# Kernel tuning notes

Measured on AMD Instinct MI355X. Metric: run time of the kernel, lower is better.

## Reference

```python
import jax, jax.numpy as jnp
import numpy as np

EMBED_DIM = 1024
NUM_HEADS = 16
HEAD_DIM = EMBED_DIM // NUM_HEADS
B, N = 2, 2048
BIAS_S = 32


def _interp_matrix(n, s):
    # Bilinear interpolation (align_corners=True) along one axis as an (n, s) matrix.
    pos = jnp.arange(n, dtype=jnp.float32) * ((s - 1) / (n - 1))
    i0 = jnp.floor(pos).astype(jnp.int32)
    i1 = jnp.minimum(i0 + 1, s - 1)
    frac = pos - i0.astype(jnp.float32)
    rows = jnp.arange(n)
    M = jnp.zeros((n, s), dtype=jnp.float32)
    M = M.at[rows, i0].add(1.0 - frac).at[rows, i1].add(frac)
    return M


def setup_inputs() -> dict:
    key = jax.random.key(0)
    ks = jax.random.split(key, 12)
    std = 0.02
    d = {
        'x': jax.random.normal(ks[0], (B, N, EMBED_DIM), dtype=jnp.float32),
        'Wq': jax.random.normal(ks[1], (EMBED_DIM, EMBED_DIM), dtype=jnp.float32) * std,
        'bq': jnp.zeros((EMBED_DIM,), dtype=jnp.float32),
        'Wk': jax.random.normal(ks[2], (EMBED_DIM, EMBED_DIM), dtype=jnp.float32) * std,
        'bk': jnp.zeros((EMBED_DIM,), dtype=jnp.float32),
        'Wv': jax.random.normal(ks[3], (EMBED_DIM, EMBED_DIM), dtype=jnp.float32) * std,
        'bv': jnp.zeros((EMBED_DIM,), dtype=jnp.float32),
        'Wo': jax.random.normal(ks[4], (EMBED_DIM, EMBED_DIM), dtype=jnp.float32) * std,
        'bo': jnp.zeros((EMBED_DIM,), dtype=jnp.float32),
        'gamma': jnp.ones((EMBED_DIM,), dtype=jnp.float32),
        'beta': jnp.zeros((EMBED_DIM,), dtype=jnp.float32),
        'rel_bias': jax.random.normal(ks[5], (NUM_HEADS, BIAS_S, BIAS_S), dtype=jnp.float32) * std,
    }
    return d


def reference(x, Wq, bq, Wk, bk, Wv, bv, Wo, bo, gamma, beta, rel_bias):
    Bx, Nx, C = x.shape
    H, D = NUM_HEADS, HEAD_DIM
    scale = 1.0 / jnp.sqrt(jnp.float32(D))

    # LayerNorm
    mu = jnp.mean(x, axis=-1, keepdims=True)
    var = jnp.mean(jnp.square(x - mu), axis=-1, keepdims=True)
    xn = (x - mu) * jax.lax.rsqrt(var + 1e-5) * gamma + beta

    q = (xn @ Wq.T + bq).reshape(Bx, Nx, H, D).transpose(0, 2, 1, 3)
    k = (xn @ Wk.T + bk).reshape(Bx, Nx, H, D).transpose(0, 2, 1, 3)
    v = (xn @ Wv.T + bv).reshape(Bx, Nx, H, D).transpose(0, 2, 1, 3)

    attn = jnp.einsum('bhnd,bhmd->bhnm', q, k) * scale  # [B,H,N,N]

    # Bilinear interp of rel_pos_bias (H,32,32) -> (H,N,N), align_corners=True
    M = _interp_matrix(Nx, BIAS_S)  # (N, 32)
    rel = jnp.einsum('ni,hij,mj->hnm', M, rel_bias, M)
    rel = rel.at[:, -1, :].set(0.0).at[:, :, -1].set(0.0)
    attn = attn + rel[None]

    mask = jnp.triu(jnp.ones((Nx, Nx), dtype=bool), k=1)
    attn = jnp.where(mask, -jnp.inf, attn)
    attn = jax.nn.softmax(attn, axis=-1)

    out = jnp.einsum('bhnm,bhmd->bhnd', attn, v)
    out = out.transpose(0, 2, 1, 3).reshape(Bx, Nx, C)
    out = out @ Wo.T + bo  # dropout is identity in eval mode
    return out
```

## Files before the change

### kernel.cpp

```cpp
#include <hip/hip_runtime.h>
#include <hip/hip_bf16.h>

#define EMBED 1024
#define NHEADS 16
#define HDIM 64
#define NB 2
#define NSEQ 2048
#define NTOK (NB*NSEQ)

using short8  = __attribute__((ext_vector_type(8))) short;
using short4v = __attribute__((ext_vector_type(4))) short;
using f32x4   = __attribute__((ext_vector_type(4))) float;

#define INV_LN2 1.4426950408889634f

__device__ __forceinline__ short f2bf(float x) {
  __hip_bfloat16 h = __float2bfloat16(x);
  short s;
  __builtin_memcpy(&s, &h, 2);
  return s;
}

#define GLDS16(gp, lp) __builtin_amdgcn_global_load_lds( \
    (const __attribute__((address_space(1))) unsigned int*)(const void*)(gp), \
    (__attribute__((address_space(3))) unsigned int*)(void*)(lp), 16, 0, 0)

__global__ __launch_bounds__(256) void ln_kernel(const float* __restrict__ x,
    const float* __restrict__ gamma, const float* __restrict__ beta,
    short* __restrict__ xn) {
  const int row = blockIdx.x;
  const int tid = threadIdx.x;
  const float* xr = x + (size_t)row * EMBED;
  float4 v = *(const float4*)(xr + tid * 4);
  float s  = v.x + v.y + v.z + v.w;
  float s2 = v.x*v.x + v.y*v.y + v.z*v.z + v.w*v.w;
#pragma unroll
  for (int off = 32; off; off >>= 1) {
    s  += __shfl_down(s, off);
    s2 += __shfl_down(s2, off);
  }
  __shared__ float red[8];
  const int wv = tid >> 6, ln = tid & 63;
  if (ln == 0) { red[wv] = s; red[4 + wv] = s2; }
  __syncthreads();
  s  = red[0] + red[1] + red[2] + red[3];
  s2 = red[4] + red[5] + red[6] + red[7];
  const float mu  = s * (1.0f / EMBED);
  const float var = s2 * (1.0f / EMBED) - mu * mu;
  const float inv = rsqrtf(var + 1e-5f);
  float4 g  = *(const float4*)(gamma + tid * 4);
  float4 bt = *(const float4*)(beta + tid * 4);
  short4v o;
  o[0] = f2bf((v.x - mu) * inv * g.x + bt.x);
  o[1] = f2bf((v.y - mu) * inv * g.y + bt.y);
  o[2] = f2bf((v.z - mu) * inv * g.z + bt.z);
  o[3] = f2bf((v.w - mu) * inv * g.w + bt.w);
  *(short4v*)(xn + (size_t)row * EMBED + tid * 4) = o;
}

__global__ __launch_bounds__(256) void cast4_kernel(
    const float* __restrict__ a, const float* __restrict__ b,
    const float* __restrict__ c, const float* __restrict__ d,
    short* __restrict__ oa, short* __restrict__ ob,
    short* __restrict__ oc, short* __restrict__ od) {
  const int wsel = blockIdx.y;
  const float* s = (wsel == 0) ? a : (wsel == 1) ? b : (wsel == 2) ? c : d;
  short* o       = (wsel == 0) ? oa : (wsel == 1) ? ob : (wsel == 2) ? oc : od;
  const int i = (blockIdx.x * 256 + threadIdx.x) * 4;
  float4 v = *(const float4*)(s + i);
  short4v r;
  r[0] = f2bf(v.x); r[1] = f2bf(v.y); r[2] = f2bf(v.z); r[3] = f2bf(v.w);
  *(short4v*)(o + i) = r;
}

template<bool F32OUT>
__global__ __launch_bounds__(256) void gemm_kernel(
    const short* __restrict__ A,
    const short* __restrict__ W0, const short* __restrict__ W1, const short* __restrict__ W2,
    const float* __restrict__ b0, const float* __restrict__ b1, const float* __restrict__ b2,
    void* __restrict__ O0, void* __restrict__ O1, void* __restrict__ O2) {
  constexpr int K = 1024, NOUT = 1024;
  const int z = blockIdx.z;
  const short* Bw   = (z == 0) ? W0 : (z == 1) ? W1 : W2;
  const float* bias = (z == 0) ? b0 : (z == 1) ? b1 : b2;
  void* Cout        = (z == 0) ? O0 : (z == 1) ? O1 : O2;

  const int tn = blockIdx.x, tm = blockIdx.y;
  const int tid = threadIdx.x, w = tid >> 6, lane = tid & 63;
  const int wm = w >> 1, wn = w & 1;
  const int g = lane >> 4, c = lane & 15;

  __shared__ short As[128 * 32];
  __shared__ short Bs[128 * 32];

  f32x4 acc[4][4];
#pragma unroll
  for (int i = 0; i < 4; i++)
#pragma unroll
    for (int j = 0; j < 4; j++) acc[i][j] = (f32x4){0.f, 0.f, 0.f, 0.f};

  const int crow = tid >> 2;
  const int ckc  = tid & 3;
  const short* ga = A  + (size_t)(tm * 128 + crow) * K + ckc * 8;
  const short* gb = Bw + (size_t)(tn * 128 + crow) * K + ckc * 8;
  short* la = &As[tid * 8];
  short* lb = &Bs[tid * 8];

  for (int k0 = 0; k0 < K; k0 += 32) {
    __syncthreads();
    GLDS16(ga + k0, la);
    GLDS16(ga + k0 + (size_t)64 * K, la + 64 * 32);
    GLDS16(gb + k0, lb);
    GLDS16(gb + k0 + (size_t)64 * K, lb + 64 * 32);
    __syncthreads();
    short8 af[4], bfr[4];
#pragma unroll
    for (int mi = 0; mi < 4; mi++)
      af[mi] = *(const short8*)&As[(wm * 64 + mi * 16 + c) * 32 + g * 8];
#pragma unroll
    for (int ni = 0; ni < 4; ni++)
      bfr[ni] = *(const short8*)&Bs[(wn * 64 + ni * 16 + c) * 32 + g * 8];
#pragma unroll
    for (int mi = 0; mi < 4; mi++)
#pragma unroll
      for (int ni = 0; ni < 4; ni++)
        acc[mi][ni] = __builtin_amdgcn_mfma_f32_16x16x32_bf16(af[mi], bfr[ni], acc[mi][ni], 0, 0, 0);
  }

#pragma unroll
  for (int ni = 0; ni < 4; ni++) {
    const int col = tn * 128 + wn * 64 + ni * 16 + c;
    const float bs = bias[col];
#pragma unroll
    for (int mi = 0; mi < 4; mi++) {
#pragma unroll
      for (int j = 0; j < 4; j++) {
        const int row = tm * 128 + wm * 64 + mi * 16 + g * 4 + j;
        const float v = acc[mi][ni][j] + bs;
        if constexpr (F32OUT)
          ((float*)Cout)[(size_t)row * NOUT + col] = v;
        else
          ((short*)Cout)[(size_t)row * NOUT + col] = f2bf(v);
      }
    }
  }
}

__global__ __launch_bounds__(256) void vtrans_kernel(const short* __restrict__ vb,
                                                     short* __restrict__ vt) {
  const int n0 = blockIdx.x * 64;
  const int bh = blockIdx.y;
  const int b = bh >> 4, h = bh & 15;
  const int tid = threadIdx.x;
  __shared__ short tl[64 * 68];

  const int r  = tid >> 3;
  const int c8 = (tid & 7) * 8;
#pragma unroll
  for (int i = 0; i < 2; i++) {
    const int row = r + i * 32;
    short8 v = *(const short8*)(vb + (size_t)(b * NSEQ + n0 + row) * EMBED + h * 64 + c8);
    *(short8*)&tl[row * 68 + c8] = v;
  }
  __syncthreads();
  const int d  = tid >> 2;
  const int ns = (tid & 3) * 16;
  short8 o0, o1;
#pragma unroll
  for (int e = 0; e < 8; e++) {
    o0[e] = tl[(ns + e) * 68 + d];
    o1[e] = tl[(ns + 8 + e) * 68 + d];
  }
  short* dst = vt + ((size_t)((b * 16 + h) * 64 + d)) * 2048 + n0 + ns;
  *(short8*)dst = o0;
  *(short8*)(dst + 8) = o1;
}

__global__ __launch_bounds__(512, 4) void attn_kernel(
    const short* __restrict__ Qm, const short* __restrict__ Km, const short* __restrict__ Vt,
    const float* __restrict__ relb, short* __restrict__ ctx) {
  const int bid = blockIdx.x;
  const int bh  = bid & 31;
  const int idx = bid >> 5;
  const int qpair = (idx < 8) ? (15 - idx) : (idx - 8);
  const int b = bh >> 4, h = bh & 15;
  const int tid = threadIdx.x, w = tid >> 6, lane = tid & 63;
  const int g = lane >> 4, c = lane & 15;
  constexpr float S31 = 31.0f / 2047.0f;
  constexpr float CSC = 0.125f * INV_LN2;

  __shared__ short k_lds[2][64 * 64];
  __shared__ short vt_lds[2][64 * 64];
  __shared__ short p_lds[8][16 * 64];
  __shared__ short rbf[128 * 32];
  __shared__ short u_lds[2][64 * 40];

  const int qbase = qpair * 128;
  const size_t bhq = (size_t)b * NSEQ * EMBED + h * HDIM;
  const short* vtb = Vt + (size_t)((b << 4) + h) * 64 * 2048;

  short8 qf[2];
  {
    const short* qp = Qm + bhq + (size_t)(qbase + w * 16 + c) * EMBED;
    qf[0] = *(const short8*)(qp + g * 8);
    qf[1] = *(const short8*)(qp + 32 + g * 8);
  }

  const int srow = tid >> 3;
  const int sd0  = (tid & 7) * 8;
  const int swz  = (srow & 7) << 3;

  auto buildU = [&](int buf, int kv) {
    if (tid < 64) {
      short* ur = &u_lds[buf][tid * 40];
      *(int4*)&ur[0]  = (int4){0, 0, 0, 0};
      *(int4*)&ur[8]  = (int4){0, 0, 0, 0};
      *(int4*)&ur[16] = (int4){0, 0, 0, 0};
      *(int4*)&ur[24] = (int4){0, 0, 0, 0};
      const int m = kv + tid;
      if (m != NSEQ - 1) {
        const float pos = m * S31;
        const int i0 = (int)pos;
        const float fr = pos - (float)i0;
        ur[i0]     = f2bf(1.0f - fr);
        ur[i0 + 1] = f2bf(fr);
      }
    }
  };

  GLDS16(Km + bhq + (size_t)srow * EMBED + (sd0 ^ swz), &k_lds[0][srow * 64 + sd0]);
  GLDS16(vtb + (size_t)srow * 2048 + (sd0 ^ swz),       &vt_lds[0][srow * 64 + sd0]);
  for (int i = tid; i < 128 * 32; i += 512) {
    const int qr = i >> 5, jj = i & 31;
    const int qg0 = qbase + qr;
    float rv = 0.f;
    if (qg0 != NSEQ - 1) {
      const float pos = qg0 * S31;
      const int i0 = (int)pos;
      const int i1 = min(i0 + 1, 31);
      const float fr = pos - (float)i0;
      const float* T = relb + h * 1024;
      rv = ((1.f - fr) * T[i0 * 32 + jj] + fr * T[i1 * 32 + jj]) * 8.0f;
    }
    rbf[i] = f2bf(rv);
  }
  buildU(0, 0);
  __syncthreads();

  const short8 rq = *(const short8*)&rbf[(w * 16 + c) * 32 + g * 8];

  float mrow = -3.0e38f, lrow = 0.f;
  f32x4 oacc[4];
#pragma unroll
  for (int db = 0; db < 4; db++) oacc[db] = (f32x4){0.f, 0.f, 0.f, 0.f};

  const int qg  = qbase + w * 16 + c;
  const int qhi = qbase + w * 16 + 15;
  const int csw = (c & 7) << 3;
  const int nkv = 2 * qpair + 2;

  for (int kt = 0; kt < nkv; kt++) {
    const int cur = kt & 1;
    const int kv0 = kt * 64;

    if (kt + 1 < nkv) {
      GLDS16(Km + bhq + (size_t)(kv0 + 64 + srow) * EMBED + (sd0 ^ swz),
             &k_lds[cur ^ 1][srow * 64 + sd0]);
      GLDS16(vtb + (size_t)srow * 2048 + (kv0 + 64) + (sd0 ^ swz),
             &vt_lds[cur ^ 1][srow * 64 + sd0]);
      buildU(cur ^ 1, kv0 + 64);
    }

    if (kv0 <= qhi) {
      const short* kl = &k_lds[cur][0];
      const short* vl = &vt_lds[cur][0];
      const short* ul = &u_lds[cur][0];

      f32x4 st[4];
#pragma unroll
      for (int mb = 0; mb < 4; mb++) st[mb] = (f32x4){0.f, 0.f, 0.f, 0.f};
      __builtin_amdgcn_s_setprio(1);
#pragma unroll
      for (int kh = 0; kh < 2; kh++) {
        const int dk = kh * 32 + g * 8;
#pragma unroll
        for (int mb = 0; mb < 4; mb++) {
          const int row = mb * 16 + c;
          short8 kf = *(const short8*)&kl[row * 64 + (dk ^ ((row & 7) << 3))];
          st[mb] = __builtin_amdgcn_mfma_f32_16x16x32_bf16(kf, qf[kh], st[mb], 0, 0, 0);
        }
      }
#pragma unroll
      for (int mb = 0; mb < 4; mb++) {
        short8 uf = *(const short8*)&ul[(mb * 16 + c) * 40 + g * 8];
        st[mb] = __builtin_amdgcn_mfma_f32_16x16x32_bf16(uf, rq, st[mb], 0, 0, 0);
      }
      __builtin_amdgcn_s_setprio(0);

      const bool diag = (kv0 + 63 > qg);
      if (diag) {
#pragma unroll
        for (int mb = 0; mb < 4; mb++)
#pragma unroll
          for (int j = 0; j < 4; j++) {
            const int mg = kv0 + mb * 16 + g * 4 + j;
            if (mg > qg) st[mb][j] = -1.0e38f;
          }
      }
      float pmr = -3.0e38f;
#pragma unroll
      for (int mb = 0; mb < 4; mb++)
#pragma unroll
        for (int j = 0; j < 4; j++) pmr = fmaxf(pmr, st[mb][j]);
      float pmax = pmr * CSC;
      pmax = fmaxf(pmax, __shfl_xor(pmax, 16));
      pmax = fmaxf(pmax, __shfl_xor(pmax, 32));

      if (!__all(pmax - mrow <= 11.6f)) {
        const float mnew = fmaxf(mrow, pmax);
        const float al = exp2f(mrow - mnew);
        mrow = mnew;
        lrow *= al;
        float alj[4];
#pragma unroll
        for (int j = 0; j < 4; j++) alj[j] = __shfl(al, g * 4 + j);
#pragma unroll
        for (int db = 0; db < 4; db++)
#pragma unroll
          for (int j = 0; j < 4; j++) oacc[db][j] *= alj[j];
      }

      float p[4][4];
      float rs = 0.f;
#pragma unroll
      for (int mb = 0; mb < 4; mb++)
#pragma unroll
        for (int j = 0; j < 4; j++) {
          const float pe = exp2f(fmaf(st[mb][j], CSC, -mrow));
          p[mb][j] = pe;
          rs += pe;
        }
      rs += __shfl_xor(rs, 16);
      rs += __shfl_xor(rs, 32);
      lrow += rs;

      short* pw = &p_lds[w][0];
#pragma unroll
      for (int mb = 0; mb < 4; mb++)
#pragma unroll
        for (int jh = 0; jh < 2; jh++) {
          const int m = mb * 16 + g * 4 + jh * 2;
          unsigned int pk = ((unsigned int)(unsigned short)f2bf(p[mb][jh * 2 + 1]) << 16)
                          |  (unsigned int)(unsigned short)f2bf(p[mb][jh * 2]);
          *(unsigned int*)&pw[c * 64 + (m ^ csw)] = pk;
        }

      __builtin_amdgcn_s_setprio(1);
#pragma unroll
      for (int kb = 0; kb < 2; kb++) {
        const int m0 = kb * 32 + g * 8;
        short8 pa = *(const short8*)&pw[c * 64 + (m0 ^ csw)];
#pragma unroll
        for (int db = 0; db < 4; db++) {
          const int d = db * 16 + c;
          short8 vf = *(const short8*)&vl[d * 64 + (m0 ^ ((d & 7) << 3))];
          oacc[db] = __builtin_amdgcn_mfma_f32_16x16x32_bf16(pa, vf, oacc[db], 0, 0, 0);
        }
      }
      __builtin_amdgcn_s_setprio(0);
    }
    __syncthreads();
  }

  float linv[4];
#pragma unroll
  for (int j = 0; j < 4; j++) linv[j] = 1.f / __shfl(lrow, g * 4 + j);
#pragma unroll
  for (int j = 0; j < 4; j++) {
    short* op = ctx + bhq + (size_t)(qbase + w * 16 + g * 4 + j) * EMBED;
#pragma unroll
    for (int db = 0; db < 4; db++)
      op[db * 16 + c] = f2bf(oacc[db][j] * linv[j]);
  }
}

extern "C" void kernel_launch(void* const* d_in, const int* in_sizes, int n_in,
                              void* d_out, int out_size, void* d_ws, size_t ws_size,
                              hipStream_t stream) {
  const float* x     = (const float*)d_in[0];
  const float* Wq    = (const float*)d_in[1];
  const float* bq    = (const float*)d_in[2];
  const float* Wk    = (const float*)d_in[3];
  const float* bk    = (const float*)d_in[4];
  const float* Wv    = (const float*)d_in[5];
  const float* bv    = (const float*)d_in[6];
  const float* Wo    = (const float*)d_in[7];
  const float* bo    = (const float*)d_in[8];
  const float* gamma = (const float*)d_in[9];
  const float* beta  = (const float*)d_in[10];
  const float* relb  = (const float*)d_in[11];
  float* out = (float*)d_out;

  char* ws = (char*)d_ws;
  short* xn  = (short*)ws; ws += (size_t)NTOK * EMBED * 2;
  short* wqb = (short*)ws; ws += (size_t)EMBED * EMBED * 2;
  short* wkb = (short*)ws; ws += (size_t)EMBED * EMBED * 2;
  short* wvb = (short*)ws; ws += (size_t)EMBED * EMBED * 2;
  short* wob = (short*)ws; ws += (size_t)EMBED * EMBED * 2;
  short* qb  = (short*)ws; ws += (size_t)NTOK * EMBED * 2;
  short* kb_ = (short*)ws; ws += (size_t)NTOK * EMBED * 2;
  short* vb  = (short*)ws; ws += (size_t)NTOK * EMBED * 2;
  short* ctx = (short*)ws; ws += (size_t)NTOK * EMBED * 2;
  short* vtb = xn;

  ln_kernel<<<dim3(NTOK), dim3(256), 0, stream>>>(x, gamma, beta, xn);
  cast4_kernel<<<dim3(1024, 4), dim3(256), 0, stream>>>(Wq, Wk, Wv, Wo, wqb, wkb, wvb, wob);
  gemm_kernel<false><<<dim3(8, 32, 3), dim3(256), 0, stream>>>(
      xn, wqb, wkb, wvb, bq, bk, bv, (void*)qb, (void*)kb_, (void*)vb);
  vtrans_kernel<<<dim3(32, 32), dim3(256), 0, stream>>>(vb, vtb);
  attn_kernel<<<dim3(512), dim3(512), 0, stream>>>(qb, kb_, vtb, relb, ctx);
  gemm_kernel<true><<<dim3(8, 32, 1), dim3(256), 0, stream>>>(
      ctx, wob, wob, wob, bo, bo, bo, (void*)out, (void*)out, (void*)out);
}
```

Measured before the change: 217.7 us.

## Fuse LayerNorm with weight casts and add a pipelined 256x256 QKV GEMM

Merges the LayerNorm and weight bf16-cast kernels into one launch. Replaces the 128x128 QKV GEMM with a 512-thread, 256x256-tile kernel. The new kernel double-buffers LDS using direct global-to-LDS loads with XOR swizzling, interleaves MFMA phases with s_setprio, and applies a block-index swizzle. The larger tile raises arithmetic intensity and hides load latency, but it needs 128KB of LDS and launches only 192 blocks, which may underfill the GPU's CUs.

```diff
diff --git a/kernel.cpp b/kernel.cpp
--- a/kernel.cpp
+++ b/kernel.cpp
@@ -25,66 +25,200 @@
     (const __attribute__((address_space(1))) unsigned int*)(const void*)(gp), \
     (__attribute__((address_space(3))) unsigned int*)(void*)(lp), 16, 0, 0)
 
-__global__ __launch_bounds__(256) void ln_kernel(const float* __restrict__ x,
-    const float* __restrict__ gamma, const float* __restrict__ beta,
-    short* __restrict__ xn) {
-  const int row = blockIdx.x;
+#define BAR() __builtin_amdgcn_s_barrier()
+#define WAITVM(N) asm volatile("s_waitcnt vmcnt(" #N ")" ::: "memory")
+#define PH_SYNC1() do { BAR(); \
+    asm volatile("s_waitcnt lgkmcnt(0)" ::: "memory"); \
+    __builtin_amdgcn_sched_barrier(0); \
+    __builtin_amdgcn_s_setprio(1); } while (0)
+#define PH_SYNC2() do { __builtin_amdgcn_s_setprio(0); BAR(); } while (0)
+
+__global__ __launch_bounds__(256) void lncast_kernel(const float* __restrict__ x,
+    const float* __restrict__ gamma, const float* __restrict__ beta, short* __restrict__ xn,
+    const float* __restrict__ Wq, const float* __restrict__ Wk,
+    const float* __restrict__ Wv, const float* __restrict__ Wo,
+    short* __restrict__ wqb, short* __restrict__ wkb,
+    short* __restrict__ wvb, short* __restrict__ wob) {
+  const int bid = blockIdx.x;
   const int tid = threadIdx.x;
-  const float* xr = x + (size_t)row * EMBED;
-  float4 v = *(const float4*)(xr + tid * 4);
-  float s  = v.x + v.y + v.z + v.w;
-  float s2 = v.x*v.x + v.y*v.y + v.z*v.z + v.w*v.w;
-#pragma unroll
-  for (int off = 32; off; off >>= 1) {
-    s  += __shfl_down(s, off);
-    s2 += __shfl_down(s2, off);
-  }
-  __shared__ float red[8];
-  const int wv = tid >> 6, ln = tid & 63;
-  if (ln == 0) { red[wv] = s; red[4 + wv] = s2; }
-  __syncthreads();
-  s  = red[0] + red[1] + red[2] + red[3];
-  s2 = red[4] + red[5] + red[6] + red[7];
-  const float mu  = s * (1.0f / EMBED);
-  const float var = s2 * (1.0f / EMBED) - mu * mu;
-  const float inv = rsqrtf(var + 1e-5f);
-  float4 g  = *(const float4*)(gamma + tid * 4);
-  float4 bt = *(const float4*)(beta + tid * 4);
-  short4v o;
-  o[0] = f2bf((v.x - mu) * inv * g.x + bt.x);
-  o[1] = f2bf((v.y - mu) * inv * g.y + bt.y);
-  o[2] = f2bf((v.z - mu) * inv * g.z + bt.z);
-  o[3] = f2bf((v.w - mu) * inv * g.w + bt.w);
-  *(short4v*)(xn + (size_t)row * EMBED + tid * 4) = o;
-}
-
-__global__ __launch_bounds__(256) void cast4_kernel(
-    const float* __restrict__ a, const float* __restrict__ b,
-    const float* __restrict__ c, const float* __restrict__ d,
-    short* __restrict__ oa, short* __restrict__ ob,
-    short* __restrict__ oc, short* __restrict__ od) {
-  const int wsel = blockIdx.y;
-  const float* s = (wsel == 0) ? a : (wsel == 1) ? b : (wsel == 2) ? c : d;
-  short* o       = (wsel == 0) ? oa : (wsel == 1) ? ob : (wsel == 2) ? oc : od;
-  const int i = (blockIdx.x * 256 + threadIdx.x) * 4;
-  float4 v = *(const float4*)(s + i);
-  short4v r;
-  r[0] = f2bf(v.x); r[1] = f2bf(v.y); r[2] = f2bf(v.z); r[3] = f2bf(v.w);
-  *(short4v*)(o + i) = r;
-}
-
-template<bool F32OUT>
-__global__ __launch_bounds__(256) void gemm_kernel(
+  if (bid < NTOK) {
+    const float* xr = x + (size_t)bid * EMBED;
+    float4 v = *(const float4*)(xr + tid * 4);
+    float s  = v.x + v.y + v.z + v.w;
+    float s2 = v.x*v.x + v.y*v.y + v.z*v.z + v.w*v.w;
+#pragma unroll
+    for (int off = 32; off; off >>= 1) {
+      s  += __shfl_down(s, off);
+      s2 += __shfl_down(s2, off);
+    }
+    __shared__ float red[8];
+    const int wv = tid >> 6, ln = tid & 63;
+    if (ln == 0) { red[wv] = s; red[4 + wv] = s2; }
+    __syncthreads();
+    s  = red[0] + red[1] + red[2] + red[3];
+    s2 = red[4] + red[5] + red[6] + red[7];
+    const float mu  = s * (1.0f / EMBED);
+    const float var = s2 * (1.0f / EMBED) - mu * mu;
+    const float inv = rsqrtf(var + 1e-5f);
+    float4 g  = *(const float4*)(gamma + tid * 4);
+    float4 bt = *(const float4*)(beta + tid * 4);
+    short4v o;
+    o[0] = f2bf((v.x - mu) * inv * g.x + bt.x);
+    o[1] = f2bf((v.y - mu) * inv * g.y + bt.y);
+    o[2] = f2bf((v.z - mu) * inv * g.z + bt.z);
+    o[3] = f2bf((v.w - mu) * inv * g.w + bt.w);
+    *(short4v*)(xn + (size_t)bid * EMBED + tid * 4) = o;
+  } else {
+    const int i = (bid - NTOK) * 1024 + tid * 4;
+    const int wsel = i >> 20;
+    const int off  = i & 1048575;
+    const float* s = (wsel == 0) ? Wq : (wsel == 1) ? Wk : (wsel == 2) ? Wv : Wo;
+    short* o       = (wsel == 0) ? wqb : (wsel == 1) ? wkb : (wsel == 2) ? wvb : wob;
+    float4 v = *(const float4*)(s + off);
+    short4v r;
+    r[0] = f2bf(v.x); r[1] = f2bf(v.y); r[2] = f2bf(v.z); r[3] = f2bf(v.w);
+    *(short4v*)(o + off) = r;
+  }
+}
+
+__global__ __launch_bounds__(512, 2) void qkv8_kernel(
     const short* __restrict__ A,
     const short* __restrict__ W0, const short* __restrict__ W1, const short* __restrict__ W2,
     const float* __restrict__ b0, const float* __restrict__ b1, const float* __restrict__ b2,
-    void* __restrict__ O0, void* __restrict__ O1, void* __restrict__ O2) {
+    short* __restrict__ O0, short* __restrict__ O1, short* __restrict__ O2) {
+  constexpr int K = 1024;
+  const int orig = blockIdx.x;
+  const int swzb = (orig & 7) * 24 + (orig >> 3);
+  const int tn = swzb % 12, tm = swzb / 12;
+  const int sel = tn >> 2;
+  const short* Bw   = (sel == 0) ? W0 : (sel == 1) ? W1 : W2;
+  const float* bias = (sel == 0) ? b0 : (sel == 1) ? b1 : b2;
+  short* Cout       = (sel == 0) ? O0 : (sel == 1) ? O1 : O2;
+  const int ncol0 = (tn & 3) * 256;
+
+  const int tid = threadIdx.x;
+  const int w = tid >> 6, lane = tid & 63;
+  const int wr = w >> 2, wc = w & 3;
+  const int g = lane >> 4, c = lane & 15;
+
+  __shared__ short As[2][256 * 64];
+  __shared__ short Bs[2][256 * 64];
+
+  f32x4 acc[8][4];
+#pragma unroll
+  for (int i = 0; i < 8; i++)
+#pragma unroll
+    for (int j = 0; j < 4; j++) acc[i][j] = (f32x4){0.f, 0.f, 0.f, 0.f};
+
+  const int sr  = tid >> 3;
+  const int sc8 = (tid & 7) * 8;
+  const int ssw = (sr & 7) << 3;
+  const short* ga = A  + (size_t)(tm * 256) * K;
+  const short* gb = Bw + (size_t)ncol0 * K;
+
+  auto stA = [&](int buf, int h, int kt) {
+#pragma unroll
+    for (int i = 0; i < 2; i++) {
+      const int row = h * 64 + i * 128 + sr;
+      GLDS16(ga + (size_t)row * K + kt * 64 + (sc8 ^ ssw), &As[buf][row * 64 + sc8]);
+    }
+  };
+  auto stB = [&](int buf, int h, int kt) {
+#pragma unroll
+    for (int i = 0; i < 2; i++) {
+      const int row = ((sr >> 5) + 2 * i) * 64 + (sr & 31) + h * 32;
+      GLDS16(gb + (size_t)row * K + kt * 64 + (sc8 ^ ssw), &Bs[buf][row * 64 + sc8]);
+    }
+  };
+
+  short8 af[4][2], bf[4][2];
+  auto ldA = [&](const short* as, int mh) {
+#pragma unroll
+    for (int mi = 0; mi < 4; mi++) {
+      const int row = wr * 128 + mh * 64 + mi * 16 + c;
+      const int sw = (row & 7) << 3;
+#pragma unroll
+      for (int ks = 0; ks < 2; ks++)
+        af[mi][ks] = *(const short8*)&as[row * 64 + ((ks * 32 + g * 8) ^ sw)];
+    }
+  };
+  auto ldB = [&](const short* bs) {
+#pragma unroll
+    for (int ni = 0; ni < 4; ni++) {
+      const int row = wc * 64 + ni * 16 + c;
+      const int sw = (row & 7) << 3;
+#pragma unroll
+      for (int ks = 0; ks < 2; ks++)
+        bf[ni][ks] = *(const short8*)&bs[row * 64 + ((ks * 32 + g * 8) ^ sw)];
+    }
+  };
+  auto MF = [&](int mh, int nh) {
+#pragma unroll
+    for (int ks = 0; ks < 2; ks++)
+#pragma unroll
+      for (int mi = 0; mi < 4; mi++)
+#pragma unroll
+        for (int ni = 0; ni < 2; ni++)
+          acc[mh * 4 + mi][nh * 2 + ni] = __builtin_amdgcn_mfma_f32_16x16x32_bf16(
+              af[mi][ks], bf[nh * 2 + ni][ks], acc[mh * 4 + mi][nh * 2 + ni], 0, 0, 0);
+  };
+
+  stA(0, 0, 0); stB(0, 0, 0); stA(0, 1, 0); stB(0, 1, 0);
+  stA(1, 0, 1); stB(1, 0, 1);
+  WAITVM(4);
+  BAR();
+
+  for (int i = 0; i < 8; ++i) {
+    const bool pre = (i < 7);
+    const int e2 = 2 * i + 2, o1 = 2 * i + 1, o3 = 2 * i + 3;
+    ldA(As[0], 0); ldB(Bs[0]);
+    stA(1, 1, o1);
+    PH_SYNC1(); MF(0, 0); PH_SYNC2();
+    stB(1, 1, o1);
+    PH_SYNC1(); MF(0, 1); PH_SYNC2();
+    ldA(As[0], 1);
+    if (pre) stA(0, 0, e2);
+    PH_SYNC1(); MF(1, 0); PH_SYNC2();
+    if (pre) stB(0, 0, e2);
+    PH_SYNC1(); MF(1, 1);
+    __builtin_amdgcn_s_setprio(0);
+    if (pre) { WAITVM(4); } else { WAITVM(0); }
+    BAR();
+    ldA(As[1], 0); ldB(Bs[1]);
+    if (pre) stA(0, 1, e2);
+    PH_SYNC1(); MF(0, 0); PH_SYNC2();
+    if (pre) stB(0, 1, e2);
+    PH_SYNC1(); MF(0, 1); PH_SYNC2();
+    ldA(As[1], 1);
+    if (pre) stA(1, 0, o3);
+    PH_SYNC1(); MF(1, 0); PH_SYNC2();
+    if (pre) stB(1, 0, o3);
+    PH_SYNC1(); MF(1, 1);
+    __builtin_amdgcn_s_setprio(0);
+    if (pre) WAITVM(4);
+    BAR();
+  }
+
+#pragma unroll
+  for (int ni4 = 0; ni4 < 4; ni4++) {
+    const int lcol = ncol0 + wc * 64 + ni4 * 16 + c;
+    const float bsv = bias[lcol];
+#pragma unroll
+    for (int mi8 = 0; mi8 < 8; mi8++) {
+      const int mo = (mi8 >> 2) * 64 + (mi8 & 3) * 16;
+      const int row = tm * 256 + wr * 128 + mo + g * 4;
+#pragma unroll
+      for (int j = 0; j < 4; j++)
+        Cout[(size_t)(row + j) * 1024 + lcol] = f2bf(acc[mi8][ni4][j] + bsv);
+    }
+  }
+}
+
+template<bool F32OUT>
+__global__ __launch_bounds__(256) void gemm_kernel(
+    const short* __restrict__ A, const short* __restrict__ Bw,
+    const float* __restrict__ bias, void* __restrict__ Cout) {
   constexpr int K = 1024, NOUT = 1024;
-  const int z = blockIdx.z;
-  const short* Bw   = (z == 0) ? W0 : (z == 1) ? W1 : W2;
-  const float* bias = (z == 0) ? b0 : (z == 1) ? b1 : b2;
-  void* Cout        = (z == 0) ? O0 : (z == 1) ? O1 : O2;
-
   const int tn = blockIdx.x, tm = blockIdx.y;
   const int tid = threadIdx.x, w = tid >> 6, lane = tid & 63;
   const int wm = w >> 1, wn = w & 1;
@@ -413,12 +547,11 @@
   short* ctx = (short*)ws; ws += (size_t)NTOK * EMBED * 2;
   short* vtb = xn;
 
-  ln_kernel<<<dim3(NTOK), dim3(256), 0, stream>>>(x, gamma, beta, xn);
-  cast4_kernel<<<dim3(1024, 4), dim3(256), 0, stream>>>(Wq, Wk, Wv, Wo, wqb, wkb, wvb, wob);
-  gemm_kernel<false><<<dim3(8, 32, 3), dim3(256), 0, stream>>>(
-      xn, wqb, wkb, wvb, bq, bk, bv, (void*)qb, (void*)kb_, (void*)vb);
+  lncast_kernel<<<dim3(NTOK + 4096), dim3(256), 0, stream>>>(
+      x, gamma, beta, xn, Wq, Wk, Wv, Wo, wqb, wkb, wvb, wob);
+  qkv8_kernel<<<dim3(192), dim3(512), 0, stream>>>(
+      xn, wqb, wkb, wvb, bq, bk, bv, qb, kb_, vb);
   vtrans_kernel<<<dim3(32, 32), dim3(256), 0, stream>>>(vb, vtb);
   attn_kernel<<<dim3(512), dim3(512), 0, stream>>>(qb, kb_, vtb, relb, ctx);
-  gemm_kernel<true><<<dim3(8, 32, 1), dim3(256), 0, stream>>>(
-      ctx, wob, wob, wob, bo, bo, bo, (void*)out, (void*)out, (void*)out);
-}
+  gemm_kernel<true><<<dim3(8, 32), dim3(256), 0, stream>>>(ctx, wob, bo, (void*)out);
+}
```

After: 213.6 us. Within noise of the previous version (-1.9%).

## Fuse LN with weight cast and rewrite QKV GEMM as double-buffered concatenated tile

Applied to the files above, without the earlier changes.

Merges the LayerNorm and fp32-to-bf16 weight cast into a single launch. Replaces the three-way z-indexed QKV GEMM with one kernel over a concatenated 3072-wide weight. That kernel uses 128x192 tiles, 512 threads, 64-wide K steps with double-buffered global-to-LDS loads, an XOR swizzle against bank conflicts, and block-index swizzling for cache locality. It aims to cut launch overhead and improve MFMA utilization and data reuse, at the cost of higher LDS usage per block.

```diff
diff --git a/kernel.cpp b/kernel.cpp
--- a/kernel.cpp
+++ b/kernel.cpp
@@ -25,66 +25,150 @@
     (const __attribute__((address_space(1))) unsigned int*)(const void*)(gp), \
     (__attribute__((address_space(3))) unsigned int*)(void*)(lp), 16, 0, 0)
 
-__global__ __launch_bounds__(256) void ln_kernel(const float* __restrict__ x,
-    const float* __restrict__ gamma, const float* __restrict__ beta,
-    short* __restrict__ xn) {
-  const int row = blockIdx.x;
+__global__ __launch_bounds__(256) void lncast_kernel(const float* __restrict__ x,
+    const float* __restrict__ gamma, const float* __restrict__ beta, short* __restrict__ xn,
+    const float* __restrict__ Wq, const float* __restrict__ Wk,
+    const float* __restrict__ Wv, const float* __restrict__ Wo,
+    short* __restrict__ wqb, short* __restrict__ wkb,
+    short* __restrict__ wvb, short* __restrict__ wob) {
+  const int bid = blockIdx.x;
   const int tid = threadIdx.x;
-  const float* xr = x + (size_t)row * EMBED;
-  float4 v = *(const float4*)(xr + tid * 4);
-  float s  = v.x + v.y + v.z + v.w;
-  float s2 = v.x*v.x + v.y*v.y + v.z*v.z + v.w*v.w;
-#pragma unroll
-  for (int off = 32; off; off >>= 1) {
-    s  += __shfl_down(s, off);
-    s2 += __shfl_down(s2, off);
-  }
-  __shared__ float red[8];
-  const int wv = tid >> 6, ln = tid & 63;
-  if (ln == 0) { red[wv] = s; red[4 + wv] = s2; }
+  if (bid < NTOK) {
+    const float* xr = x + (size_t)bid * EMBED;
+    float4 v = *(const float4*)(xr + tid * 4);
+    float s  = v.x + v.y + v.z + v.w;
+    float s2 = v.x*v.x + v.y*v.y + v.z*v.z + v.w*v.w;
+#pragma unroll
+    for (int off = 32; off; off >>= 1) {
+      s  += __shfl_down(s, off);
+      s2 += __shfl_down(s2, off);
+    }
+    __shared__ float red[8];
+    const int wv = tid >> 6, ln = tid & 63;
+    if (ln == 0) { red[wv] = s; red[4 + wv] = s2; }
+    __syncthreads();
+    s  = red[0] + red[1] + red[2] + red[3];
+    s2 = red[4] + red[5] + red[6] + red[7];
+    const float mu  = s * (1.0f / EMBED);
+    const float var = s2 * (1.0f / EMBED) - mu * mu;
+    const float inv = rsqrtf(var + 1e-5f);
+    float4 g  = *(const float4*)(gamma + tid * 4);
+    float4 bt = *(const float4*)(beta + tid * 4);
+    short4v o;
+    o[0] = f2bf((v.x - mu) * inv * g.x + bt.x);
+    o[1] = f2bf((v.y - mu) * inv * g.y + bt.y);
+    o[2] = f2bf((v.z - mu) * inv * g.z + bt.z);
+    o[3] = f2bf((v.w - mu) * inv * g.w + bt.w);
+    *(short4v*)(xn + (size_t)bid * EMBED + tid * 4) = o;
+  } else {
+    const int i = (bid - NTOK) * 1024 + tid * 4;
+    const int wsel = i >> 20;
+    const int off  = i & 1048575;
+    const float* s = (wsel == 0) ? Wq : (wsel == 1) ? Wk : (wsel == 2) ? Wv : Wo;
+    short* o       = (wsel == 0) ? wqb : (wsel == 1) ? wkb : (wsel == 2) ? wvb : wob;
+    float4 v = *(const float4*)(s + off);
+    short4v r;
+    r[0] = f2bf(v.x); r[1] = f2bf(v.y); r[2] = f2bf(v.z); r[3] = f2bf(v.w);
+    *(short4v*)(o + off) = r;
+  }
+}
+
+__global__ __launch_bounds__(512, 4) void qkv2ph_kernel(
+    const short* __restrict__ A, const short* __restrict__ Wcat,
+    const float* __restrict__ b0, const float* __restrict__ b1, const float* __restrict__ b2,
+    short* __restrict__ O0, short* __restrict__ O1, short* __restrict__ O2) {
+  constexpr int K = 1024;
+  const int orig = blockIdx.x;
+  const int swzb = (orig & 7) * 64 + (orig >> 3);
+  const int tn = swzb & 15, tm = swzb >> 4;
+
+  const int tid = threadIdx.x;
+  const int w = tid >> 6, lane = tid & 63;
+  const int wr = w >> 2, wc = w & 3;
+  const int g = lane >> 4, c = lane & 15;
+
+  __shared__ short As[2][128 * 64];
+  __shared__ short Bs[2][192 * 64];
+
+  f32x4 acc[4][3];
+#pragma unroll
+  for (int i = 0; i < 4; i++)
+#pragma unroll
+    for (int j = 0; j < 3; j++) acc[i][j] = (f32x4){0.f, 0.f, 0.f, 0.f};
+
+  const int sr  = tid >> 3;
+  const int sc8 = (tid & 7) * 8;
+  const int ssw = (sr & 7) << 3;
+  const short* ga = A    + (size_t)(tm * 128) * K;
+  const short* gb = Wcat + (size_t)(tn * 192) * K;
+
+  auto STAGE = [&](int buf, int kt) {
+#pragma unroll
+    for (int u = 0; u < 2; u++) {
+      const int row = u * 64 + sr;
+      GLDS16(ga + (size_t)row * K + kt * 64 + (sc8 ^ ssw), &As[buf][row * 64 + sc8]);
+    }
+#pragma unroll
+    for (int u = 0; u < 3; u++) {
+      const int row = u * 64 + sr;
+      GLDS16(gb + (size_t)row * K + kt * 64 + (sc8 ^ ssw), &Bs[buf][row * 64 + sc8]);
+    }
+  };
+
+  STAGE(0, 0);
   __syncthreads();
-  s  = red[0] + red[1] + red[2] + red[3];
-  s2 = red[4] + red[5] + red[6] + red[7];
-  const float mu  = s * (1.0f / EMBED);
-  const float var = s2 * (1.0f / EMBED) - mu * mu;
-  const float inv = rsqrtf(var + 1e-5f);
-  float4 g  = *(const float4*)(gamma + tid * 4);
-  float4 bt = *(const float4*)(beta + tid * 4);
-  short4v o;
-  o[0] = f2bf((v.x - mu) * inv * g.x + bt.x);
-  o[1] = f2bf((v.y - mu) * inv * g.y + bt.y);
-  o[2] = f2bf((v.z - mu) * inv * g.z + bt.z);
-  o[3] = f2bf((v.w - mu) * inv * g.w + bt.w);
-  *(short4v*)(xn + (size_t)row * EMBED + tid * 4) = o;
-}
-
-__global__ __launch_bounds__(256) void cast4_kernel(
-    const float* __restrict__ a, const float* __restrict__ b,
-    const float* __restrict__ c, const float* __restrict__ d,
-    short* __restrict__ oa, short* __restrict__ ob,
-    short* __restrict__ oc, short* __restrict__ od) {
-  const int wsel = blockIdx.y;
-  const float* s = (wsel == 0) ? a : (wsel == 1) ? b : (wsel == 2) ? c : d;
-  short* o       = (wsel == 0) ? oa : (wsel == 1) ? ob : (wsel == 2) ? oc : od;
-  const int i = (blockIdx.x * 256 + threadIdx.x) * 4;
-  float4 v = *(const float4*)(s + i);
-  short4v r;
-  r[0] = f2bf(v.x); r[1] = f2bf(v.y); r[2] = f2bf(v.z); r[3] = f2bf(v.w);
-  *(short4v*)(o + i) = r;
+
+  for (int kt = 0; kt < 16; ++kt) {
+    const int cur = kt & 1;
+    if (kt + 1 < 16) STAGE(cur ^ 1, kt + 1);
+    const short* as = As[cur];
+    const short* bs = Bs[cur];
+#pragma unroll
+    for (int ks = 0; ks < 2; ks++) {
+      short8 af[4], bf[3];
+#pragma unroll
+      for (int mi = 0; mi < 4; mi++) {
+        const int row = wr * 64 + mi * 16 + c;
+        af[mi] = *(const short8*)&as[row * 64 + ((ks * 32 + g * 8) ^ ((row & 7) << 3))];
+      }
+#pragma unroll
+      for (int ni = 0; ni < 3; ni++) {
+        const int row = wc * 48 + ni * 16 + c;
+        bf[ni] = *(const short8*)&bs[row * 64 + ((ks * 32 + g * 8) ^ ((row & 7) << 3))];
+      }
+      __builtin_amdgcn_s_setprio(1);
+#pragma unroll
+      for (int mi = 0; mi < 4; mi++)
+#pragma unroll
+        for (int ni = 0; ni < 3; ni++)
+          acc[mi][ni] = __builtin_amdgcn_mfma_f32_16x16x32_bf16(af[mi], bf[ni], acc[mi][ni], 0, 0, 0);
+      __builtin_amdgcn_s_setprio(0);
+    }
+    __syncthreads();
+  }
+
+#pragma unroll
+  for (int ni = 0; ni < 3; ni++) {
+    const int col = tn * 192 + wc * 48 + ni * 16 + c;
+    const int sel = col >> 10, lc = col & 1023;
+    short* O        = (sel == 0) ? O0 : (sel == 1) ? O1 : O2;
+    const float* bb = (sel == 0) ? b0 : (sel == 1) ? b1 : b2;
+    const float bsv = bb[lc];
+#pragma unroll
+    for (int mi = 0; mi < 4; mi++) {
+      const int row = tm * 128 + wr * 64 + mi * 16 + g * 4;
+#pragma unroll
+      for (int j = 0; j < 4; j++)
+        O[(size_t)(row + j) * 1024 + lc] = f2bf(acc[mi][ni][j] + bsv);
+    }
+  }
 }
 
 template<bool F32OUT>
 __global__ __launch_bounds__(256) void gemm_kernel(
-    const short* __restrict__ A,
-    const short* __restrict__ W0, const short* __restrict__ W1, const short* __restrict__ W2,
-    const float* __restrict__ b0, const float* __restrict__ b1, const float* __restrict__ b2,
-    void* __restrict__ O0, void* __restrict__ O1, void* __restrict__ O2) {
+    const short* __restrict__ A, const short* __restrict__ Bw,
+    const float* __restrict__ bias, void* __restrict__ Cout) {
   constexpr int K = 1024, NOUT = 1024;
-  const int z = blockIdx.z;
-  const short* Bw   = (z == 0) ? W0 : (z == 1) ? W1 : W2;
-  const float* bias = (z == 0) ? b0 : (z == 1) ? b1 : b2;
-  void* Cout        = (z == 0) ? O0 : (z == 1) ? O1 : O2;
-
   const int tn = blockIdx.x, tm = blockIdx.y;
   const int tid = threadIdx.x, w = tid >> 6, lane = tid & 63;
   const int wm = w >> 1, wn = w & 1;
@@ -413,12 +497,11 @@
   short* ctx = (short*)ws; ws += (size_t)NTOK * EMBED * 2;
   short* vtb = xn;
 
-  ln_kernel<<<dim3(NTOK), dim3(256), 0, stream>>>(x, gamma, beta, xn);
-  cast4_kernel<<<dim3(1024, 4), dim3(256), 0, stream>>>(Wq, Wk, Wv, Wo, wqb, wkb, wvb, wob);
-  gemm_kernel<false><<<dim3(8, 32, 3), dim3(256), 0, stream>>>(
-      xn, wqb, wkb, wvb, bq, bk, bv, (void*)qb, (void*)kb_, (void*)vb);
+  lncast_kernel<<<dim3(NTOK + 4096), dim3(256), 0, stream>>>(
+      x, gamma, beta, xn, Wq, Wk, Wv, Wo, wqb, wkb, wvb, wob);
+  qkv2ph_kernel<<<dim3(512), dim3(512), 0, stream>>>(
+      xn, wqb, bq, bk, bv, qb, kb_, vb);
   vtrans_kernel<<<dim3(32, 32), dim3(256), 0, stream>>>(vb, vtb);
   attn_kernel<<<dim3(512), dim3(512), 0, stream>>>(qb, kb_, vtb, relb, ctx);
-  gemm_kernel<true><<<dim3(8, 32, 1), dim3(256), 0, stream>>>(
-      ctx, wob, wob, wob, bo, bo, bo, (void*)out, (void*)out, (void*)out);
-}
+  gemm_kernel<true><<<dim3(8, 32), dim3(256), 0, stream>>>(ctx, wob, bo, (void*)out);
+}
```

Measured after the change: 211.5 us. 1.03x faster.
